# Optimization experiments

Hardware: AMD Instinct MI355X
Metric: run time of the kernel (lower is better)

## Reference

```python
import jax, jax.numpy as jnp
import numpy as np

N_NODES = 50000
N_EDGES = 600000
IN_DIM = 128
HID = 128
N_CLASSES = 40
N_GRAPHS = 128


def setup_inputs() -> dict:
    key = jax.random.key(0)
    ks = jax.random.split(key, 12)
    x = jax.random.normal(ks[0], (N_NODES, IN_DIM), dtype=jnp.float32)
    edge_index = jax.random.randint(ks[1], (2, N_EDGES), 0, N_NODES, dtype=jnp.int64)
    batch = jnp.sort(jax.random.randint(ks[2], (N_NODES,), 0, N_GRAPHS, dtype=jnp.int64))
    dims = [IN_DIM, HID, HID, N_CLASSES]
    params = {}
    for l in range(3):
        d_in, d_out = dims[l], dims[l + 1]
        s = 1.0 / np.sqrt(d_in)
        params[f"Wl{l}"] = jax.random.uniform(ks[3 + 3 * l], (d_out, d_in), jnp.float32, -s, s)
        params[f"bl{l}"] = jax.random.uniform(ks[4 + 3 * l], (d_out,), jnp.float32, -s, s)
        params[f"Wr{l}"] = jax.random.uniform(ks[5 + 3 * l], (d_out, d_in), jnp.float32, -s, s)
    return {"x": x, "edge_index": edge_index, "batch": batch, **params}


def _sage_layer(h, src, dst, Wl, bl, Wr):
    # message: relu(x_j) (edge_attr is None -> zero), mean-aggregate at dst
    m = jnp.maximum(h[src], 0.0)                       # [E, d]
    agg = jax.ops.segment_sum(m, dst, num_segments=N_NODES)
    cnt = jax.ops.segment_sum(jnp.ones((m.shape[0],), h.dtype), dst, num_segments=N_NODES)
    agg = agg / jnp.maximum(cnt, 1.0)[:, None]
    # lin_l(agg) + lin_r(x)
    return agg @ Wl.T + bl + h @ Wr.T


def reference(x, edge_index, batch, Wl0, bl0, Wr0, Wl1, bl1, Wr1, Wl2, bl2, Wr2):
    src, dst = edge_index[0], edge_index[1]
    Ws = [(Wl0, bl0, Wr0), (Wl1, bl1, Wr1), (Wl2, bl2, Wr2)]
    h = x
    for l, (Wl, bl, Wr) in enumerate(Ws):
        # dropout is identity in eval mode
        h = _sage_layer(h, src, dst, Wl, bl, Wr)
        if l != len(Ws) - 1:
            h = jnp.maximum(h, 0.0)
    # global mean pool over graphs
    gsum = jax.ops.segment_sum(h, batch, num_segments=N_GRAPHS)
    gcnt = jax.ops.segment_sum(jnp.ones((h.shape[0],), h.dtype), batch, num_segments=N_GRAPHS)
    g = gsum / jnp.maximum(gcnt, 1.0)[:, None]
    return h, g
```

## Files before the change

### kernel.cpp

```cpp
#include <hip/hip_runtime.h>
#include <hip/hip_bf16.h>


#define NODES 50000
#define K_DIM 128
#define N_GRAPHS 128

typedef __attribute__((ext_vector_type(8))) short short8;
typedef __attribute__((ext_vector_type(4))) short short4v;
typedef __attribute__((ext_vector_type(4))) float f32x4;

__device__ inline short f2bf(float f) {
    unsigned u = __builtin_bit_cast(unsigned, f);
    u += 0x7FFFu + ((u >> 16) & 1u);
    return (short)(u >> 16);
}
__device__ inline float bf2f(short h) {
    unsigned u = ((unsigned)(unsigned short)h) << 16;
    return __builtin_bit_cast(float, u);
}
__device__ inline float blo(unsigned u) { return __builtin_bit_cast(float, u << 16); }
__device__ inline float bhi(unsigned u) { return __builtin_bit_cast(float, u & 0xFFFF0000u); }
__device__ inline unsigned hilo_pack(float f) {
    short h = f2bf(f);
    short l = f2bf(f - bf2f(h));
    return ((unsigned)(unsigned short)h) | (((unsigned)(unsigned short)l) << 16);
}

__global__ void init_kernel(const float* __restrict__ w0, const float* __restrict__ w1,
                            const float* __restrict__ w2, const float* __restrict__ w3,
                            const float* __restrict__ w4, const float* __restrict__ w5,
                            short* __restrict__ whi, short* __restrict__ wlo,
                            int* __restrict__ deg, const int* __restrict__ batch,
                            int* __restrict__ gstart, int* __restrict__ counter,
                            const float* __restrict__ x, short* __restrict__ xb,
                            float* __restrict__ gsum, int N) {
    int idx = blockIdx.x * 256 + threadIdx.x;
    if (idx < N * (K_DIM / 4)) {
        float4 v = reinterpret_cast<const float4*>(x)[idx];
        short4v b;
        b[0] = f2bf(fmaxf(v.x, 0.f));
        b[1] = f2bf(fmaxf(v.y, 0.f));
        b[2] = f2bf(fmaxf(v.z, 0.f));
        b[3] = f2bf(fmaxf(v.w, 0.f));
        *reinterpret_cast<short4v*>(&xb[idx * 4]) = b;
    }
    if (idx < N) deg[idx] = 0;
    if (idx < N_GRAPHS * 40) gsum[idx] = 0.f;
    if (idx == 0) *counter = 0;
    const int TOT = 4 * 16384 + 96 * 128;
    if (idx < TOT) {
        float v;
        if (idx < 65536) {
            int m = idx >> 14, e = idx & 16383;
            const float* W = (m == 0) ? w0 : (m == 1) ? w1 : (m == 2) ? w2 : w3;
            v = W[e];
        } else {
            int i2 = idx - 65536;
            int row = i2 >> 7, col = i2 & 127;
            if (row < 40)      v = w4[row * 128 + col];
            else if (row < 80) v = w5[(row - 40) * 128 + col];
            else               v = 0.f;
        }
        unsigned p = hilo_pack(v);
        whi[idx] = (short)(p & 0xFFFFu);
        wlo[idx] = (short)(p >> 16);
    }
    if (idx <= N_GRAPHS) {
        int g = idx;
        int lo = 0, hi = N;
        while (lo < hi) {
            int mid = (lo + hi) >> 1;
            if (batch[mid] < g) lo = mid + 1; else hi = mid;
        }
        gstart[g] = lo;
    }
}

__global__ void deg_kernel(const int* __restrict__ dst, int* __restrict__ deg, int E) {
    int e = blockIdx.x * blockDim.x + threadIdx.x;
    if (e < E) atomicAdd(&deg[dst[e]], 1);
}

__global__ void csr_offsets(const int* __restrict__ deg, int* __restrict__ counter,
                            int* __restrict__ rowptr, int* __restrict__ fillpos, int N) {
    const int tid = threadIdx.x, lane = tid & 63, wv = tid >> 6;
    int i = blockIdx.x * 256 + tid;
    int v = (i < N) ? deg[i] : 0;
    int incl = v;
    #pragma unroll
    for (int off = 1; off < 64; off <<= 1) {
        int t = __shfl_up(incl, off, 64);
        if (lane >= off) incl += t;
    }
    __shared__ int ws[4];
    __shared__ int sbase;
    if (lane == 63) ws[wv] = incl;
    __syncthreads();
    if (tid == 0) sbase = atomicAdd(counter, ws[0] + ws[1] + ws[2] + ws[3]);
    __syncthreads();
    int add = sbase;
    for (int k = 0; k < wv; ++k) add += ws[k];
    int excl = add + incl - v;
    if (i < N) { rowptr[i] = excl; fillpos[i] = excl; }
}

__global__ void fill_kernel(const int* __restrict__ src, const int* __restrict__ dst,
                            int* __restrict__ fillpos, int* __restrict__ csr_src, int E) {
    int e = blockIdx.x * blockDim.x + threadIdx.x;
    if (e < E) {
        int p = atomicAdd(&fillpos[dst[e]], 1);
        csr_src[p] = src[e];
    }
}

__global__ void agg_bf16(const unsigned short* __restrict__ hb,
                         const int* __restrict__ rowptr, const int* __restrict__ deg,
                         const int* __restrict__ csr_src,
                         short* __restrict__ aggb, int N) {
    int w = (blockIdx.x * blockDim.x + threadIdx.x) >> 6;
    if (w >= N) return;
    int lane = threadIdx.x & 63;
    int slot = lane >> 4, l16 = lane & 15;
    int s = rowptr[w];
    int e = s + deg[w];
    const uint4* T = reinterpret_cast<const uint4*>(hb);
    float2 a0 = make_float2(0.f, 0.f), a1 = a0, a2 = a0, a3 = a0;
    int i = s + slot;
    for (; i + 4 < e; i += 8) {
        uint4 va = T[(size_t)csr_src[i] * 16 + l16];
        uint4 vb = T[(size_t)csr_src[i + 4] * 16 + l16];
        a0.x += blo(va.x) + blo(vb.x); a0.y += bhi(va.x) + bhi(vb.x);
        a1.x += blo(va.y) + blo(vb.y); a1.y += bhi(va.y) + bhi(vb.y);
        a2.x += blo(va.z) + blo(vb.z); a2.y += bhi(va.z) + bhi(vb.z);
        a3.x += blo(va.w) + blo(vb.w); a3.y += bhi(va.w) + bhi(vb.w);
    }
    for (; i < e; i += 4) {
        uint4 va = T[(size_t)csr_src[i] * 16 + l16];
        a0.x += blo(va.x); a0.y += bhi(va.x);
        a1.x += blo(va.y); a1.y += bhi(va.y);
        a2.x += blo(va.z); a2.y += bhi(va.z);
        a3.x += blo(va.w); a3.y += bhi(va.w);
    }
    #pragma unroll
    for (int off = 16; off <= 32; off <<= 1) {
        a0.x += __shfl_xor(a0.x, off, 64); a0.y += __shfl_xor(a0.y, off, 64);
        a1.x += __shfl_xor(a1.x, off, 64); a1.y += __shfl_xor(a1.y, off, 64);
        a2.x += __shfl_xor(a2.x, off, 64); a2.y += __shfl_xor(a2.y, off, 64);
        a3.x += __shfl_xor(a3.x, off, 64); a3.y += __shfl_xor(a3.y, off, 64);
    }
    if (slot == 0) {
        float inv = 1.0f / fmaxf((float)(e - s), 1.0f);
        short8 b;
        b[0] = f2bf(a0.x * inv); b[1] = f2bf(a0.y * inv);
        b[2] = f2bf(a1.x * inv); b[3] = f2bf(a1.y * inv);
        b[4] = f2bf(a2.x * inv); b[5] = f2bf(a2.y * inv);
        b[6] = f2bf(a3.x * inv); b[7] = f2bf(a3.y * inv);
        *reinterpret_cast<short8*>(&aggb[(size_t)w * K_DIM + l16 * 8]) = b;
    }
}

__global__ __launch_bounds__(256) void sage0_mfma(
        const short* __restrict__ Ab_in, const float* __restrict__ Xf,
        const short* __restrict__ Bhl, const short* __restrict__ Bll,
        const short* __restrict__ Bhr, const short* __restrict__ Blr,
        const float* __restrict__ bl,
        short* __restrict__ outHi, short* __restrict__ outLo, int N) {
    constexpr int BM = 64;
    constexpr int LSTR = 40;
    const int tid = threadIdx.x;
    const int lane = tid & 63;
    const int wave = tid >> 6;
    const int l15 = lane & 15;
    const int quad = lane >> 4;
    const int m0 = blockIdx.x * BM;
    const int srow = tid >> 2, sc8 = tid & 3;

    __shared__ __align__(16) short Ab [BM * LSTR];
    __shared__ __align__(16) short Ahi[BM * LSTR];
    __shared__ __align__(16) short Alo[BM * LSTR];

    f32x4 acc[4][2];
    #pragma unroll
    for (int i = 0; i < 4; ++i)
        #pragma unroll
        for (int j = 0; j < 2; ++j) acc[i][j] = (f32x4){0.f, 0.f, 0.f, 0.f};

    const short8 zero8 = (short8){0, 0, 0, 0, 0, 0, 0, 0};
    const int sm = m0 + srow;

    for (int k0 = 0; k0 < K_DIM; k0 += 32) {
        __syncthreads();
        {
            short8 va = zero8, vh = zero8, vl = zero8;
            if (sm < N) {
                va = *reinterpret_cast<const short8*>(Ab_in + (size_t)sm * K_DIM + k0 + sc8 * 8);
                const float* xp = Xf + (size_t)sm * K_DIM + k0 + sc8 * 8;
                float4 f0 = *reinterpret_cast<const float4*>(xp);
                float4 f1 = *reinterpret_cast<const float4*>(xp + 4);
                float fv[8] = {f0.x, f0.y, f0.z, f0.w, f1.x, f1.y, f1.z, f1.w};
                #pragma unroll
                for (int j = 0; j < 8; ++j) {
                    unsigned p = hilo_pack(fv[j]);
                    vh[j] = (short)(p & 0xFFFFu);
                    vl[j] = (short)(p >> 16);
                }
            }
            *reinterpret_cast<short8*>(&Ab [srow * LSTR + sc8 * 8]) = va;
            *reinterpret_cast<short8*>(&Ahi[srow * LSTR + sc8 * 8]) = vh;
            *reinterpret_cast<short8*>(&Alo[srow * LSTR + sc8 * 8]) = vl;
        }
        short8 bhl_[2], bll_[2], bhr_[2], blr_[2];
        #pragma unroll
        for (int nt = 0; nt < 2; ++nt) {
            int n = wave * 32 + nt * 16 + l15;
            size_t off = (size_t)n * K_DIM + k0 + quad * 8;
            bhl_[nt] = *reinterpret_cast<const short8*>(Bhl + off);
            bll_[nt] = *reinterpret_cast<const short8*>(Bll + off);
            bhr_[nt] = *reinterpret_cast<const short8*>(Bhr + off);
            blr_[nt] = *reinterpret_cast<const short8*>(Blr + off);
        }
        __syncthreads();
        #pragma unroll
        for (int mt = 0; mt < 4; ++mt) {
            int row = mt * 16 + l15;
            short8 ab = *reinterpret_cast<const short8*>(&Ab [row * LSTR + quad * 8]);
            short8 ah = *reinterpret_cast<const short8*>(&Ahi[row * LSTR + quad * 8]);
            short8 ao = *reinterpret_cast<const short8*>(&Alo[row * LSTR + quad * 8]);
            #pragma unroll
            for (int nt = 0; nt < 2; ++nt) {
                acc[mt][nt] = __builtin_amdgcn_mfma_f32_16x16x32_bf16(ab, bhl_[nt], acc[mt][nt], 0, 0, 0);
                acc[mt][nt] = __builtin_amdgcn_mfma_f32_16x16x32_bf16(ab, bll_[nt], acc[mt][nt], 0, 0, 0);
                acc[mt][nt] = __builtin_amdgcn_mfma_f32_16x16x32_bf16(ah, bhr_[nt], acc[mt][nt], 0, 0, 0);
                acc[mt][nt] = __builtin_amdgcn_mfma_f32_16x16x32_bf16(ah, blr_[nt], acc[mt][nt], 0, 0, 0);
                acc[mt][nt] = __builtin_amdgcn_mfma_f32_16x16x32_bf16(ao, bhr_[nt], acc[mt][nt], 0, 0, 0);
            }
        }
    }

    #pragma unroll
    for (int mt = 0; mt < 4; ++mt) {
        #pragma unroll
        for (int nt = 0; nt < 2; ++nt) {
            int col = wave * 32 + nt * 16 + l15;
            float b = bl[col];
            #pragma unroll
            for (int reg = 0; reg < 4; ++reg) {
                int row = m0 + mt * 16 + quad * 4 + reg;
                if (row < N) {
                    float v = fmaxf(acc[mt][nt][reg] + b, 0.f);
                    unsigned p = hilo_pack(v);
                    outHi[(size_t)row * K_DIM + col] = (short)(p & 0xFFFFu);
                    outLo[(size_t)row * K_DIM + col] = (short)(p >> 16);
                }
            }
        }
    }
}

__global__ __launch_bounds__(256) void sage1_gemm80(
        const short* __restrict__ Ab_in,
        const short* __restrict__ Hhi_in, const short* __restrict__ Hlo_in,
        const short* __restrict__ Bhl, const short* __restrict__ Bll,
        const short* __restrict__ Bhr, const short* __restrict__ Blr,
        const float* __restrict__ bl,
        const short* __restrict__ B2h, const short* __restrict__ B2l,
        const float* __restrict__ b2,
        short* __restrict__ ylb, float* __restrict__ yr40, int N) {
    constexpr int BM = 32;
    constexpr int LSTR = 40;
    constexpr int LSTR2 = 68;
    const int tid = threadIdx.x;
    const int lane = tid & 63;
    const int wave = tid >> 6;
    const int l15 = lane & 15;
    const int quad = lane >> 4;
    const int m0 = blockIdx.x * BM;
    const int srow = tid >> 3, sc4 = tid & 7;

    __shared__ __align__(16) short Ab [BM * LSTR];
    __shared__ __align__(16) short Ahi[BM * LSTR];
    __shared__ __align__(16) short Alo[BM * LSTR];
    __shared__ __align__(16) short H2h[BM * LSTR2];
    __shared__ __align__(16) short H2l[BM * LSTR2];

    f32x4 acc[2][2];
    #pragma unroll
    for (int i = 0; i < 2; ++i)
        #pragma unroll
        for (int j = 0; j < 2; ++j) acc[i][j] = (f32x4){0.f, 0.f, 0.f, 0.f};

    const short4v zero4 = (short4v){0, 0, 0, 0};
    const int sm = m0 + srow;
    const bool rowok = (sm < N);

    short4v va = zero4, vh = zero4, vl = zero4;
    if (rowok) {
        va = *reinterpret_cast<const short4v*>(Ab_in  + (size_t)sm * K_DIM + sc4 * 4);
        vh = *reinterpret_cast<const short4v*>(Hhi_in + (size_t)sm * K_DIM + sc4 * 4);
        vl = *reinterpret_cast<const short4v*>(Hlo_in + (size_t)sm * K_DIM + sc4 * 4);
    }

    for (int k0 = 0; k0 < K_DIM; k0 += 32) {
        short8 bhl_[2], bll_[2], bhr_[2], blr_[2];
        #pragma unroll
        for (int nt = 0; nt < 2; ++nt) {
            int n = wave * 32 + nt * 16 + l15;
            size_t off = (size_t)n * K_DIM + k0 + quad * 8;
            bhl_[nt] = *reinterpret_cast<const short8*>(Bhl + off);
            bll_[nt] = *reinterpret_cast<const short8*>(Bll + off);
            bhr_[nt] = *reinterpret_cast<const short8*>(Bhr + off);
            blr_[nt] = *reinterpret_cast<const short8*>(Blr + off);
        }
        __syncthreads();
        *reinterpret_cast<short4v*>(&Ab [srow * LSTR + sc4 * 4]) = va;
        *reinterpret_cast<short4v*>(&Ahi[srow * LSTR + sc4 * 4]) = vh;
        *reinterpret_cast<short4v*>(&Alo[srow * LSTR + sc4 * 4]) = vl;
        __syncthreads();
        if (k0 + 32 < K_DIM && rowok) {
            va = *reinterpret_cast<const short4v*>(Ab_in  + (size_t)sm * K_DIM + k0 + 32 + sc4 * 4);
            vh = *reinterpret_cast<const short4v*>(Hhi_in + (size_t)sm * K_DIM + k0 + 32 + sc4 * 4);
            vl = *reinterpret_cast<const short4v*>(Hlo_in + (size_t)sm * K_DIM + k0 + 32 + sc4 * 4);
        }
        #pragma unroll
        for (int mt = 0; mt < 2; ++mt) {
            int row = mt * 16 + l15;
            short8 ab = *reinterpret_cast<const short8*>(&Ab [row * LSTR + quad * 8]);
            short8 ah = *reinterpret_cast<const short8*>(&Ahi[row * LSTR + quad * 8]);
            short8 ao = *reinterpret_cast<const short8*>(&Alo[row * LSTR + quad * 8]);
            #pragma unroll
            for (int nt = 0; nt < 2; ++nt) {
                acc[mt][nt] = __builtin_amdgcn_mfma_f32_16x16x32_bf16(ab, bhl_[nt], acc[mt][nt], 0, 0, 0);
                acc[mt][nt] = __builtin_amdgcn_mfma_f32_16x16x32_bf16(ab, bll_[nt], acc[mt][nt], 0, 0, 0);
                acc[mt][nt] = __builtin_amdgcn_mfma_f32_16x16x32_bf16(ah, bhr_[nt], acc[mt][nt], 0, 0, 0);
                acc[mt][nt] = __builtin_amdgcn_mfma_f32_16x16x32_bf16(ah, blr_[nt], acc[mt][nt], 0, 0, 0);
                acc[mt][nt] = __builtin_amdgcn_mfma_f32_16x16x32_bf16(ao, bhr_[nt], acc[mt][nt], 0, 0, 0);
            }
        }
    }

    const int rg = wave >> 1, ch = wave & 1;
    const int NT = ch ? 2 : 3;
    const int ntb = ch ? 3 : 0;
    f32x4 c2[3];
    #pragma unroll
    for (int j = 0; j < 3; ++j) c2[j] = (f32x4){0.f, 0.f, 0.f, 0.f};
    const int arow = rg * 16 + l15;

    #pragma unroll
    for (int half = 0; half < 2; ++half) {
        __syncthreads();
        if ((wave >> 1) == half) {
            #pragma unroll
            for (int mt = 0; mt < 2; ++mt) {
                #pragma unroll
                for (int nt = 0; nt < 2; ++nt) {
                    int col = (wave & 1) * 32 + nt * 16 + l15;
                    float b = bl[half * 64 + col];
                    #pragma unroll
                    for (int reg = 0; reg < 4; ++reg) {
                        int row = mt * 16 + quad * 4 + reg;
                        float v = fmaxf(acc[mt][nt][reg] + b, 0.f);
                        unsigned p = hilo_pack(v);
                        H2h[row * LSTR2 + col] = (short)(p & 0xFFFFu);
                        H2l[row * LSTR2 + col] = (short)(p >> 16);
                    }
                }
            }
        }
        __syncthreads();
        #pragma unroll
        for (int kc2 = 0; kc2 < 2; ++kc2) {
            const int k0 = half * 64 + kc2 * 32;
            short8 ah = *reinterpret_cast<const short8*>(&H2h[arow * LSTR2 + kc2 * 32 + quad * 8]);
            short8 ao = *reinterpret_cast<const short8*>(&H2l[arow * LSTR2 + kc2 * 32 + quad * 8]);
            for (int j = 0; j < NT; ++j) {
                int n = (ntb + j) * 16 + l15;
                size_t off = (size_t)n * K_DIM + k0 + quad * 8;
                short8 bh = *reinterpret_cast<const short8*>(B2h + off);
                short8 bo = *reinterpret_cast<const short8*>(B2l + off);
                c2[j] = __builtin_amdgcn_mfma_f32_16x16x32_bf16(ah, bh, c2[j], 0, 0, 0);
                c2[j] = __builtin_amdgcn_mfma_f32_16x16x32_bf16(ah, bo, c2[j], 0, 0, 0);
                c2[j] = __builtin_amdgcn_mfma_f32_16x16x32_bf16(ao, bh, c2[j], 0, 0, 0);
            }
        }
    }

    for (int j = 0; j < NT; ++j) {
        int col = (ntb + j) * 16 + l15;
        #pragma unroll
        for (int reg = 0; reg < 4; ++reg) {
            int row = m0 + rg * 16 + quad * 4 + reg;
            if (row < N) {
                float v = c2[j][reg];
                if (col < 40) {
                    ylb[(size_t)row * 40 + col] = f2bf(v);
                } else {
                    yr40[(size_t)row * 40 + (col - 40)] = v + b2[col - 40];
                }
            }
        }
    }
}

__global__ __launch_bounds__(256) void agg40_pool(
        const unsigned int* __restrict__ ylbu, const float* __restrict__ yr40,
        const int* __restrict__ rowptr, const int* __restrict__ deg,
        const int* __restrict__ csr_src,
        const int* __restrict__ batch, const int* __restrict__ gstart,
        float* __restrict__ out, float* __restrict__ gsum, int N) {
    const int w = (blockIdx.x * blockDim.x + threadIdx.x) >> 6;
    const int lane = threadIdx.x & 63;
    const int wv = threadIdx.x >> 6;
    const int half = lane >> 5, l32 = lane & 31;
    __shared__ float sh[4][40];
    __shared__ int sg[4];
    __shared__ float sinv[4];

    if (w < N) {
        int s = rowptr[w], e = s + deg[w];
        float ax = 0.f, ay = 0.f;
        if (l32 < 20) {
            int i = s + half;
            for (; i + 6 < e; i += 8) {
                int s0 = csr_src[i], s1 = csr_src[i + 2], s2 = csr_src[i + 4], s3 = csr_src[i + 6];
                unsigned v0 = ylbu[(size_t)s0 * 20 + l32];
                unsigned v1 = ylbu[(size_t)s1 * 20 + l32];
                unsigned v2 = ylbu[(size_t)s2 * 20 + l32];
                unsigned v3 = ylbu[(size_t)s3 * 20 + l32];
                ax += (blo(v0) + blo(v1)) + (blo(v2) + blo(v3));
                ay += (bhi(v0) + bhi(v1)) + (bhi(v2) + bhi(v3));
            }
            for (; i < e; i += 2) {
                unsigned v0 = ylbu[(size_t)csr_src[i] * 20 + l32];
                ax += blo(v0); ay += bhi(v0);
            }
        }
        ax += __shfl_xor(ax, 32, 64);
        ay += __shfl_xor(ay, 32, 64);
        if (half == 0 && l32 < 20) {
            float inv = 1.0f / fmaxf((float)(e - s), 1.0f);
            float2 yr = *reinterpret_cast<const float2*>(&yr40[(size_t)w * 40 + 2 * l32]);
            float vx = ax * inv + yr.x;
            float vy = ay * inv + yr.y;
            *reinterpret_cast<float2*>(&out[(size_t)w * 40 + 2 * l32]) = make_float2(vx, vy);
            sh[wv][2 * l32]     = vx;
            sh[wv][2 * l32 + 1] = vy;
        }
    }
    if (lane == 0) {
        if (w < N) {
            int g = batch[w];
            sg[wv] = g;
            sinv[wv] = 1.0f / fmaxf((float)(gstart[g + 1] - gstart[g]), 1.0f);
        } else {
            sg[wv] = -1;
        }
    }
    __syncthreads();
    if (wv == 0 && lane < 40) {
        int cur = -1;
        float accum = 0.f;
        #pragma unroll
        for (int k = 0; k < 4; ++k) {
            int gk = sg[k];
            if (gk < 0) continue;
            float c = sh[k][lane] * sinv[k];
            if (gk == cur) {
                accum += c;
            } else {
                if (cur >= 0) atomicAdd(&gsum[cur * 40 + lane], accum);
                cur = gk;
                accum = c;
            }
        }
        if (cur >= 0) atomicAdd(&gsum[cur * 40 + lane], accum);
    }
}

extern "C" void kernel_launch(void* const* d_in, const int* in_sizes, int n_in,
                              void* d_out, int out_size, void* d_ws, size_t ws_size,
                              hipStream_t stream) {
    const float* x    = (const float*)d_in[0];
    const int*   ei   = (const int*)d_in[1];
    const int*   batch= (const int*)d_in[2];
    const float* Wl0  = (const float*)d_in[3];
    const float* bl0  = (const float*)d_in[4];
    const float* Wr0  = (const float*)d_in[5];
    const float* Wl1  = (const float*)d_in[6];
    const float* bl1  = (const float*)d_in[7];
    const float* Wr1  = (const float*)d_in[8];
    const float* Wl2  = (const float*)d_in[9];
    const float* bl2  = (const float*)d_in[10];
    const float* Wr2  = (const float*)d_in[11];

    const int N = in_sizes[0] / K_DIM;
    const int E = in_sizes[1] / 2;
    const int* src = ei;
    const int* dst = ei + E;

    float* out = (float*)d_out;
    float* gsum = out + (size_t)N * 40;

    char* w = (char*)d_ws;
    auto alloc = [&](size_t bytes) {
        char* p = w;
        w += (bytes + 255) & ~(size_t)255;
        return p;
    };
    const size_t PL = (size_t)N * K_DIM * 2;
    short* aggb  = (short*)alloc(PL);
    short* xb    = (short*)alloc(PL);
    short* h1hi  = (short*)alloc(PL);
    short* h1lo  = (short*)alloc(PL);
    short* ylb   = (short*)alloc((size_t)N * 40 * 2);
    float* yr40  = (float*)alloc((size_t)N * 40 * 4);
    int*   rowptr= (int*)alloc((size_t)(N + 1) * 4);
    int*   deg   = (int*)alloc((size_t)N * 4);
    int*   fillp = (int*)alloc((size_t)N * 4);
    int*   csr   = (int*)alloc((size_t)E * 4);
    int*   counter = (int*)alloc(256);
    int*   gstart= (int*)alloc((size_t)(N_GRAPHS + 1) * 4);
    short* whi   = (short*)alloc(77824 * 2);
    short* wlo   = (short*)alloc(77824 * 2);

    const int NB = (N + 255) / 256;
    const int initGrid = (N * (K_DIM / 4) + 255) / 256;

    init_kernel<<<initGrid, 256, 0, stream>>>(Wl0, Wr0, Wl1, Wr1, Wl2, Wr2,
                                              whi, wlo, deg, batch, gstart, counter,
                                              x, xb, gsum, N);
    deg_kernel<<<(E + 255) / 256, 256, 0, stream>>>(dst, deg, E);
    csr_offsets<<<NB, 256, 0, stream>>>(deg, counter, rowptr, fillp, N);
    fill_kernel<<<(E + 255) / 256, 256, 0, stream>>>(src, dst, fillp, csr, E);

    short* hWl0 = whi;          short* lWl0 = wlo;
    short* hWr0 = whi + 16384;  short* lWr0 = wlo + 16384;
    short* hWl1 = whi + 32768;  short* lWl1 = wlo + 32768;
    short* hWr1 = whi + 49152;  short* lWr1 = wlo + 49152;
    short* hW2  = whi + 65536;  short* lW2  = wlo + 65536;

    const int aggGrid   = (N * 64 + 255) / 256;
    const int gemmGrid  = (N + 63) / 64;
    const int gemmGrid32= (N + 31) / 32;

    agg_bf16<<<aggGrid, 256, 0, stream>>>((const unsigned short*)xb, rowptr, deg, csr, aggb, N);
    sage0_mfma<<<gemmGrid, 256, 0, stream>>>(
        aggb, x, hWl0, lWl0, hWr0, lWr0, bl0, h1hi, h1lo, N);
    agg_bf16<<<aggGrid, 256, 0, stream>>>((const unsigned short*)h1hi, rowptr, deg, csr, aggb, N);
    sage1_gemm80<<<gemmGrid32, 256, 0, stream>>>(
        aggb, h1hi, h1lo, hWl1, lWl1, hWr1, lWr1, bl1, hW2, lW2, bl2, ylb, yr40, N);
    agg40_pool<<<aggGrid, 256, 0, stream>>>((const unsigned int*)ylb, yr40,
                                            rowptr, deg, csr, batch, gstart, out, gsum, N);
}
```

Baseline: 327.1 us.

## Stage full-K A tile in LDS once and write whole hidden tile before second GEMM

The fused layer-1/layer-2 GEMM kernel now loads the entire 32x128 A, H-hi and H-lo tiles into shared memory up front with 16-byte loads, then runs all four K chunks without per-chunk barriers. The intermediate hidden tile is written in one pass by all waves into an LDS buffer that reuses the A storage, replacing the two-half staged epilogue and its extra synchronisations. This removes several __syncthreads and the serialized half-by-half hidden-tile handoff. In exchange it uses more LDS per block (about 26 KB), which may lower occupancy, and it loses the register prefetch overlap of the next A chunk.

```diff
diff --git a/kernel.cpp b/kernel.cpp
--- a/kernel.cpp
+++ b/kernel.cpp
@@ -268,21 +268,20 @@
         const float* __restrict__ b2,
         short* __restrict__ ylb, float* __restrict__ yr40, int N) {
     constexpr int BM = 32;
-    constexpr int LSTR = 40;
-    constexpr int LSTR2 = 68;
+    constexpr int LSTA = 136;
     const int tid = threadIdx.x;
     const int lane = tid & 63;
     const int wave = tid >> 6;
     const int l15 = lane & 15;
     const int quad = lane >> 4;
     const int m0 = blockIdx.x * BM;
-    const int srow = tid >> 3, sc4 = tid & 7;
-
-    __shared__ __align__(16) short Ab [BM * LSTR];
-    __shared__ __align__(16) short Ahi[BM * LSTR];
-    __shared__ __align__(16) short Alo[BM * LSTR];
-    __shared__ __align__(16) short H2h[BM * LSTR2];
-    __shared__ __align__(16) short H2l[BM * LSTR2];
+
+    __shared__ __align__(16) short SH[3 * BM * LSTA];
+    short* AbL = SH;
+    short* AhL = SH + BM * LSTA;
+    short* AlL = SH + 2 * BM * LSTA;
+    short* H2h = SH;
+    short* H2l = SH + BM * LSTA;
 
     f32x4 acc[2][2];
     #pragma unroll
@@ -290,18 +289,36 @@
         #pragma unroll
         for (int j = 0; j < 2; ++j) acc[i][j] = (f32x4){0.f, 0.f, 0.f, 0.f};
 
-    const short4v zero4 = (short4v){0, 0, 0, 0};
-    const int sm = m0 + srow;
-    const bool rowok = (sm < N);
-
-    short4v va = zero4, vh = zero4, vl = zero4;
-    if (rowok) {
-        va = *reinterpret_cast<const short4v*>(Ab_in  + (size_t)sm * K_DIM + sc4 * 4);
-        vh = *reinterpret_cast<const short4v*>(Hhi_in + (size_t)sm * K_DIM + sc4 * 4);
-        vl = *reinterpret_cast<const short4v*>(Hlo_in + (size_t)sm * K_DIM + sc4 * 4);
-    }
-
-    for (int k0 = 0; k0 < K_DIM; k0 += 32) {
+    const short8 zero8 = (short8){0, 0, 0, 0, 0, 0, 0, 0};
+
+    {
+        const int srow = tid >> 3;
+        const int c0 = (tid & 7) * 16;
+        const int sm = m0 + srow;
+        short8 a0 = zero8, a1 = zero8, h0 = zero8, h1 = zero8, l0 = zero8, l1 = zero8;
+        if (sm < N) {
+            const short* pa = Ab_in  + (size_t)sm * K_DIM + c0;
+            const short* ph = Hhi_in + (size_t)sm * K_DIM + c0;
+            const short* pl = Hlo_in + (size_t)sm * K_DIM + c0;
+            a0 = *reinterpret_cast<const short8*>(pa);
+            a1 = *reinterpret_cast<const short8*>(pa + 8);
+            h0 = *reinterpret_cast<const short8*>(ph);
+            h1 = *reinterpret_cast<const short8*>(ph + 8);
+            l0 = *reinterpret_cast<const short8*>(pl);
+            l1 = *reinterpret_cast<const short8*>(pl + 8);
+        }
+        *reinterpret_cast<short8*>(&AbL[srow * LSTA + c0])     = a0;
+        *reinterpret_cast<short8*>(&AbL[srow * LSTA + c0 + 8]) = a1;
+        *reinterpret_cast<short8*>(&AhL[srow * LSTA + c0])     = h0;
+        *reinterpret_cast<short8*>(&AhL[srow * LSTA + c0 + 8]) = h1;
+        *reinterpret_cast<short8*>(&AlL[srow * LSTA + c0])     = l0;
+        *reinterpret_cast<short8*>(&AlL[srow * LSTA + c0 + 8]) = l1;
+    }
+    __syncthreads();
+
+    #pragma unroll
+    for (int kc = 0; kc < 4; ++kc) {
+        const int k0 = kc * 32;
         short8 bhl_[2], bll_[2], bhr_[2], blr_[2];
         #pragma unroll
         for (int nt = 0; nt < 2; ++nt) {
@@ -312,22 +329,12 @@
             bhr_[nt] = *reinterpret_cast<const short8*>(Bhr + off);
             blr_[nt] = *reinterpret_cast<const short8*>(Blr + off);
         }
-        __syncthreads();
-        *reinterpret_cast<short4v*>(&Ab [srow * LSTR + sc4 * 4]) = va;
-        *reinterpret_cast<short4v*>(&Ahi[srow * LSTR + sc4 * 4]) = vh;
-        *reinterpret_cast<short4v*>(&Alo[srow * LSTR + sc4 * 4]) = vl;
-        __syncthreads();
-        if (k0 + 32 < K_DIM && rowok) {
-            va = *reinterpret_cast<const short4v*>(Ab_in  + (size_t)sm * K_DIM + k0 + 32 + sc4 * 4);
-            vh = *reinterpret_cast<const short4v*>(Hhi_in + (size_t)sm * K_DIM + k0 + 32 + sc4 * 4);
-            vl = *reinterpret_cast<const short4v*>(Hlo_in + (size_t)sm * K_DIM + k0 + 32 + sc4 * 4);
-        }
         #pragma unroll
         for (int mt = 0; mt < 2; ++mt) {
             int row = mt * 16 + l15;
-            short8 ab = *reinterpret_cast<const short8*>(&Ab [row * LSTR + quad * 8]);
-            short8 ah = *reinterpret_cast<const short8*>(&Ahi[row * LSTR + quad * 8]);
-            short8 ao = *reinterpret_cast<const short8*>(&Alo[row * LSTR + quad * 8]);
+            short8 ab = *reinterpret_cast<const short8*>(&AbL[row * LSTA + k0 + quad * 8]);
+            short8 ah = *reinterpret_cast<const short8*>(&AhL[row * LSTA + k0 + quad * 8]);
+            short8 ao = *reinterpret_cast<const short8*>(&AlL[row * LSTA + k0 + quad * 8]);
             #pragma unroll
             for (int nt = 0; nt < 2; ++nt) {
                 acc[mt][nt] = __builtin_amdgcn_mfma_f32_16x16x32_bf16(ab, bhl_[nt], acc[mt][nt], 0, 0, 0);
@@ -339,6 +346,26 @@
         }
     }
 
+    __syncthreads();
+
+    #pragma unroll
+    for (int mt = 0; mt < 2; ++mt) {
+        #pragma unroll
+        for (int nt = 0; nt < 2; ++nt) {
+            int col = wave * 32 + nt * 16 + l15;
+            float b = bl[col];
+            #pragma unroll
+            for (int reg = 0; reg < 4; ++reg) {
+                int row = mt * 16 + quad * 4 + reg;
+                float v = fmaxf(acc[mt][nt][reg] + b, 0.f);
+                unsigned p = hilo_pack(v);
+                H2h[row * LSTA + col] = (short)(p & 0xFFFFu);
+                H2l[row * LSTA + col] = (short)(p >> 16);
+            }
+        }
+    }
+    __syncthreads();
+
     const int rg = wave >> 1, ch = wave & 1;
     const int NT = ch ? 2 : 3;
     const int ntb = ch ? 3 : 0;
@@ -348,41 +375,18 @@
     const int arow = rg * 16 + l15;
 
     #pragma unroll
-    for (int half = 0; half < 2; ++half) {
-        __syncthreads();
-        if ((wave >> 1) == half) {
-            #pragma unroll
-            for (int mt = 0; mt < 2; ++mt) {
-                #pragma unroll
-                for (int nt = 0; nt < 2; ++nt) {
-                    int col = (wave & 1) * 32 + nt * 16 + l15;
-                    float b = bl[half * 64 + col];
-                    #pragma unroll
-                    for (int reg = 0; reg < 4; ++reg) {
-                        int row = mt * 16 + quad * 4 + reg;
-                        float v = fmaxf(acc[mt][nt][reg] + b, 0.f);
-                        unsigned p = hilo_pack(v);
-                        H2h[row * LSTR2 + col] = (short)(p & 0xFFFFu);
-                        H2l[row * LSTR2 + col] = (short)(p >> 16);
-                    }
-                }
-            }
-        }
-        __syncthreads();
-        #pragma unroll
-        for (int kc2 = 0; kc2 < 2; ++kc2) {
-            const int k0 = half * 64 + kc2 * 32;
-            short8 ah = *reinterpret_cast<const short8*>(&H2h[arow * LSTR2 + kc2 * 32 + quad * 8]);
-            short8 ao = *reinterpret_cast<const short8*>(&H2l[arow * LSTR2 + kc2 * 32 + quad * 8]);
-            for (int j = 0; j < NT; ++j) {
-                int n = (ntb + j) * 16 + l15;
-                size_t off = (size_t)n * K_DIM + k0 + quad * 8;
-                short8 bh = *reinterpret_cast<const short8*>(B2h + off);
-                short8 bo = *reinterpret_cast<const short8*>(B2l + off);
-                c2[j] = __builtin_amdgcn_mfma_f32_16x16x32_bf16(ah, bh, c2[j], 0, 0, 0);
-                c2[j] = __builtin_amdgcn_mfma_f32_16x16x32_bf16(ah, bo, c2[j], 0, 0, 0);
-                c2[j] = __builtin_amdgcn_mfma_f32_16x16x32_bf16(ao, bh, c2[j], 0, 0, 0);
-            }
+    for (int kc = 0; kc < 4; ++kc) {
+        const int k0 = kc * 32;
+        short8 ah = *reinterpret_cast<const short8*>(&H2h[arow * LSTA + k0 + quad * 8]);
+        short8 ao = *reinterpret_cast<const short8*>(&H2l[arow * LSTA + k0 + quad * 8]);
+        for (int j = 0; j < NT; ++j) {
+            int n = (ntb + j) * 16 + l15;
+            size_t off = (size_t)n * K_DIM + k0 + quad * 8;
+            short8 bh = *reinterpret_cast<const short8*>(B2h + off);
+            short8 bo = *reinterpret_cast<const short8*>(B2l + off);
+            c2[j] = __builtin_amdgcn_mfma_f32_16x16x32_bf16(ah, bh, c2[j], 0, 0, 0);
+            c2[j] = __builtin_amdgcn_mfma_f32_16x16x32_bf16(ah, bo, c2[j], 0, 0, 0);
+            c2[j] = __builtin_amdgcn_mfma_f32_16x16x32_bf16(ao, bh, c2[j], 0, 0, 0);
         }
     }
 
```

Result: no change. 325.4 us (-0.5%).
